# Optimization experiments

Measured on AMD Instinct MI355X. Metric: run time of the kernel, lower is better.

Reference implementation:

```python
import jax, jax.numpy as jnp
import numpy as np

ALPHA = 1.0
EPS = 1e-9
MASK_FILL = 100000.0  # large value pushes masked entries to the end of ascending sort


def setup_inputs() -> dict:
    key = jax.random.key(0)
    k1, k2, k3, k4 = jax.random.split(key, 4)
    bs, nh, n = 128, 32, 2048
    input1 = jax.random.normal(k1, (bs, 4, nh, n), dtype=jnp.float32)
    input2 = jax.random.normal(k2, (bs, 1, nh, n), dtype=jnp.float32)
    mask1 = jax.random.randint(k3, (bs, 4, nh, n), 0, 2).astype(jnp.int32)
    mask2 = jax.random.randint(k4, (bs, 1, nh, n), 0, 2).astype(jnp.int32)
    return {"input1": input1, "mask1": mask1, "input2": input2, "mask2": mask2}


def reference(input1, mask1, input2, mask2):
    # input1: (bs, 4, nh, n) scores; input2/mask2: (bs, 1, nh, n) targets/mask.
    # mask1 is unused by the original forward.
    i2 = jnp.where(mask2 > 0, input2, jnp.float32(MASK_FILL))
    idx = jnp.argsort(i2, axis=-1)                                  # (bs, 1, nh, n)
    mask_sorted = jnp.take_along_axis(mask2, idx, axis=-1).astype(jnp.float32)
    idx4 = jnp.broadcast_to(idx, input1.shape)                      # repeat over the 4 choices
    inputs_sorted = jnp.take_along_axis(input1, idx4, axis=-1)      # (bs, 4, nh, n)
    proj = jnp.exp(ALPHA * inputs_sorted) * mask_sorted             # mode='exp'
    proj_cum = jnp.cumsum(proj, axis=-1) * mask_sorted
    prob = jnp.prod((proj + EPS) / (proj_cum + EPS), axis=-1)       # (bs, 4, nh)
    return jnp.transpose(prob, (0, 2, 1))                           # (bs, nh, 4)
```

## Files before the change

kernel.cpp:

```cpp
#include <hip/hip_runtime.h>

#define N   2048
#define NT  128
#define EPK 16

typedef unsigned int u32;

__device__ __forceinline__ u32 fkey(float f) {
  u32 u = __float_as_uint(f);
  return (u & 0x80000000u) ? ~u : (u | 0x80000000u);
}

__device__ __forceinline__ u32 umin32(u32 a, u32 b) { return a < b ? a : b; }
__device__ __forceinline__ u32 umax32(u32 a, u32 b) { return a < b ? b : a; }

template <int D>
__device__ __forceinline__ u32 exch(u32 x, int lane) {
  if constexpr (D == 1) {
    return (u32)__builtin_amdgcn_update_dpp((int)x, (int)x, 0xB1, 0xF, 0xF, true);
  } else if constexpr (D == 2) {
    return (u32)__builtin_amdgcn_update_dpp((int)x, (int)x, 0x4E, 0xF, 0xF, true);
  } else if constexpr (D == 4) {
    return (u32)__builtin_amdgcn_ds_swizzle((int)x, 0x101F);
  } else if constexpr (D == 8) {
    return (u32)__builtin_amdgcn_update_dpp((int)x, (int)x, 0x128, 0xF, 0xF, true);
  } else if constexpr (D == 16) {
    return (u32)__builtin_amdgcn_ds_swizzle((int)x, 0x401F);
  } else {
    int a = (int)x, b = (int)x;
    asm("v_permlane32_swap_b32 %0, %1" : "+v"(a), "+v"(b));
    return (lane & 32) ? (u32)a : (u32)b;
  }
}

template <int D>
__device__ __forceinline__ void sh_pass(u32* kv, bool keep_min, int lane) {
#pragma unroll
  for (int m = 0; m < EPK; ++m) {
    u32 o = exch<D>(kv[m], lane);
    u32 mn = umin32(kv[m], o), mx = umax32(kv[m], o);
    kv[m] = keep_min ? mn : mx;
  }
}

#define INPASS(J, UPEXPR)                               \
  {                                                     \
    _Pragma("unroll")                                   \
    for (int m = 0; m < EPK; ++m)                       \
      if ((m & (J)) == 0) {                             \
        const bool up_ = (UPEXPR);                      \
        u32 x = kv[m], y = kv[m | (J)];                 \
        u32 mn = umin32(x, y), mx = umax32(x, y);       \
        kv[m] = up_ ? mn : mx;                          \
        kv[m | (J)] = up_ ? mx : mn;                    \
      }                                                 \
  }

__device__ __forceinline__ void stage_row(const float* __restrict__ r1,
                                          float* buf, int tid, int w) {
#pragma unroll
  for (int q = 0; q < 4; ++q) {
    const float4* src = (const float4*)r1 + (tid + 128 * q);
    char* dst = (char*)buf + q * 2048 + w * 1024;
    __builtin_amdgcn_global_load_lds(
        (const __attribute__((address_space(1))) unsigned int*)src,
        (__attribute__((address_space(3))) unsigned int*)dst, 16, 0, 0);
  }
}

__global__ __launch_bounds__(NT) void listmle_kernel(
    const float* __restrict__ input1,
    const float* __restrict__ input2,
    const int* __restrict__ mask2,
    float* __restrict__ out) {
  __shared__ __align__(16) float rowbuf[N];
  __shared__ __align__(16) u32 slab[N];
  __shared__ float hand[2];

  const int tid = threadIdx.x;
  const int lane = tid & 63;
  const int w = tid >> 6;
  const int p = blockIdx.x;
  const int b = p >> 5, h = p & 31;

  {
    const float4* i2v = (const float4*)(input2 + (size_t)p * N);
    const int4* m2v = (const int4*)(mask2 + (size_t)p * N);
#pragma unroll
    for (int q = 0; q < 4; ++q) {
      float4 vv = i2v[tid + 128 * q];
      int4 mm = m2v[tid + 128 * q];
      const u32 i0 = 4u * (u32)(tid + 128 * q);
      float vs[4] = {vv.x, vv.y, vv.z, vv.w};
      int ms[4] = {mm.x, mm.y, mm.z, mm.w};
#pragma unroll
      for (int r = 0; r < 4; ++r) {
        u32 idx = i0 + r;
        u32 key = (ms[r] > 0) ? ((fkey(vs[r]) & 0xFFFFF800u) | idx)
                              : (0xFFFFF800u | idx);
        slab[idx ^ ((idx >> 5) & 31u)] = key;
      }
    }
  }
  __syncthreads();
  u32 kv[EPK];
#pragma unroll
  for (int m = 0; m < EPK; ++m) {
    u32 idx = (u32)(w * 1024 + lane * EPK + m);
    kv[m] = slab[idx ^ ((idx >> 5) & 31u)];
  }

  stage_row(input1 + ((size_t)((b * 4 + 0) * 32 + h)) * N, rowbuf, tid, w);

  INPASS(1, (m & 2) == 0)
  INPASS(2, (m & 4) == 0) INPASS(1, (m & 4) == 0)
  INPASS(4, (m & 8) == 0) INPASS(2, (m & 8) == 0) INPASS(1, (m & 8) == 0)
  {
    const bool up = (lane & 1) == 0;
    INPASS(8, up) INPASS(4, up) INPASS(2, up) INPASS(1, up)
  }
  {
    const bool up = (lane & 2) == 0;
    sh_pass<1>(kv, ((lane & 1) == 0) == up, lane);
    INPASS(8, up) INPASS(4, up) INPASS(2, up) INPASS(1, up)
  }
  {
    const bool up = (lane & 4) == 0;
    sh_pass<2>(kv, ((lane & 2) == 0) == up, lane);
    sh_pass<1>(kv, ((lane & 1) == 0) == up, lane);
    INPASS(8, up) INPASS(4, up) INPASS(2, up) INPASS(1, up)
  }
  {
    const bool up = (lane & 8) == 0;
    sh_pass<4>(kv, ((lane & 4) == 0) == up, lane);
    sh_pass<2>(kv, ((lane & 2) == 0) == up, lane);
    sh_pass<1>(kv, ((lane & 1) == 0) == up, lane);
    INPASS(8, up) INPASS(4, up) INPASS(2, up) INPASS(1, up)
  }
  {
    const bool up = (lane & 16) == 0;
    sh_pass<8>(kv, ((lane & 8) == 0) == up, lane);
    sh_pass<4>(kv, ((lane & 4) == 0) == up, lane);
    sh_pass<2>(kv, ((lane & 2) == 0) == up, lane);
    sh_pass<1>(kv, ((lane & 1) == 0) == up, lane);
    INPASS(8, up) INPASS(4, up) INPASS(2, up) INPASS(1, up)
  }
  {
    const bool up = (lane & 32) == 0;
    sh_pass<16>(kv, ((lane & 16) == 0) == up, lane);
    sh_pass<8>(kv, ((lane & 8) == 0) == up, lane);
    sh_pass<4>(kv, ((lane & 4) == 0) == up, lane);
    sh_pass<2>(kv, ((lane & 2) == 0) == up, lane);
    sh_pass<1>(kv, ((lane & 1) == 0) == up, lane);
    INPASS(8, up) INPASS(4, up) INPASS(2, up) INPASS(1, up)
  }
  {
    const bool up = (w == 0);
    sh_pass<32>(kv, ((lane & 32) == 0) == up, lane);
    sh_pass<16>(kv, ((lane & 16) == 0) == up, lane);
    sh_pass<8>(kv, ((lane & 8) == 0) == up, lane);
    sh_pass<4>(kv, ((lane & 4) == 0) == up, lane);
    sh_pass<2>(kv, ((lane & 2) == 0) == up, lane);
    sh_pass<1>(kv, ((lane & 1) == 0) == up, lane);
    INPASS(8, up) INPASS(4, up) INPASS(2, up) INPASS(1, up)
  }
  {
    __syncthreads();
#pragma unroll
    for (int m = 0; m < EPK; ++m) slab[w * 1024 + m * 64 + lane] = kv[m];
    __syncthreads();
#pragma unroll
    for (int m = 0; m < EPK; ++m) {
      u32 o = slab[(w ^ 1) * 1024 + m * 64 + lane];
      kv[m] = (w == 0) ? umin32(kv[m], o) : umax32(kv[m], o);
    }
    __syncthreads();
    sh_pass<32>(kv, (lane & 32) == 0, lane);
    sh_pass<16>(kv, (lane & 16) == 0, lane);
    sh_pass<8>(kv, (lane & 8) == 0, lane);
    sh_pass<4>(kv, (lane & 4) == 0, lane);
    sh_pass<2>(kv, (lane & 2) == 0, lane);
    sh_pass<1>(kv, (lane & 1) == 0, lane);
    INPASS(8, true) INPASS(4, true) INPASS(2, true) INPASS(1, true)
  }

  u32 pk[EPK / 2];
#pragma unroll
  for (int t = 0; t < EPK / 2; ++t) {
    u32 a = kv[2 * t], b2 = kv[2 * t + 1];
    u32 ia = (a & 0x7FFu) | ((a < 0xFFFFF800u) ? 0x800u : 0u);
    u32 ib = (b2 & 0x7FFu) | ((b2 < 0xFFFFF800u) ? 0x800u : 0u);
    pk[t] = ia | (ib << 16);
  }

#pragma unroll
  for (int c = 0; c < 4; ++c) {
    float* buf = (c & 1) ? (float*)slab : rowbuf;
    __syncthreads();
    if (c < 3) {
      float* nbuf = (c & 1) ? rowbuf : (float*)slab;
      stage_row(input1 + ((size_t)((b * 4 + c + 1) * 32 + h)) * N, nbuf, tid, w);
    }

    float e[EPK];
    float lsum = 0.f;
#pragma unroll
    for (int m = 0; m < EPK; ++m) {
      u32 info = (pk[m >> 1] >> ((m & 1) * 16)) & 0xFFFFu;
      float v = buf[info & 0x7FFu];
      float pe = (info & 0x800u) ? __expf(v) : 0.f;
      e[m] = pe;
      lsum += pe;
    }

    float inc = lsum;
#pragma unroll
    for (int d = 1; d < 64; d <<= 1) {
      float o = __shfl_up(inc, d, 64);
      if (lane >= d) inc += o;
    }
    float excl = inc - lsum;

    if (w == 0) {
      float cum = excl;
      float prod = 1.f;
#pragma unroll
      for (int m = 0; m < EPK; ++m) {
        cum += e[m];
        u32 info = pk[m >> 1] >> ((m & 1) * 16);
        if (info & 0x800u) prod *= __fdividef(e[m] + 1e-9f, cum + 1e-9f);
      }
#pragma unroll
      for (int d = 1; d < 64; d <<= 1) prod *= __shfl_xor(prod, d, 64);
      if (lane == 63) hand[0] = inc;
      if (lane == 0) hand[1] = prod;
    }
    asm volatile("s_waitcnt lgkmcnt(0)" ::: "memory");
    __builtin_amdgcn_s_barrier();
    asm volatile("" ::: "memory");
    if (w == 1) {
      float cum = hand[0] + excl;
      float prod = 1.f;
#pragma unroll
      for (int m = 0; m < EPK; ++m) {
        cum += e[m];
        u32 info = pk[m >> 1] >> ((m & 1) * 16);
        if (info & 0x800u) prod *= __fdividef(e[m] + 1e-9f, cum + 1e-9f);
      }
#pragma unroll
      for (int d = 1; d < 64; d <<= 1) prod *= __shfl_xor(prod, d, 64);
      if (lane == 0) out[(size_t)p * 4 + c] = hand[1] * prod;
    }
  }
}

extern "C" void kernel_launch(void* const* d_in, const int* in_sizes, int n_in,
                              void* d_out, int out_size, void* d_ws, size_t ws_size,
                              hipStream_t stream) {
  const float* input1 = (const float*)d_in[0];
  const float* input2 = (const float*)d_in[2];
  const int* mask2 = (const int*)d_in[3];
  float* out = (float*)d_out;

  const int problems = 128 * 32;
  listmle_kernel<<<problems, NT, 0, stream>>>(input1, input2, mask2, out);
}
```

Baseline: 80.67 us.

## Split score rows across waves so each wave owns full sorted permutation

After the sort, the packed sorted-index pairs go through LDS so each wave holds the whole permutation, 32 entries per lane. Each wave then handles two of the four score rows independently, with its own LDS buffer and its own prefetch of the next row. This removes the per-row block barriers and the cross-wave handoff of prefix sums and partial products. In exchange each lane does twice as many exp/divide steps per row, uses more registers, and pays one extra LDS round trip for the permutation.

Result: faster. 76.38 us (-5.3%).

```diff
diff --git a/kernel.cpp b/kernel.cpp
--- a/kernel.cpp
+++ b/kernel.cpp
@@ -56,12 +56,12 @@
       }                                                 \
   }
 
-__device__ __forceinline__ void stage_row(const float* __restrict__ r1,
-                                          float* buf, int tid, int w) {
-#pragma unroll
-  for (int q = 0; q < 4; ++q) {
-    const float4* src = (const float4*)r1 + (tid + 128 * q);
-    char* dst = (char*)buf + q * 2048 + w * 1024;
+__device__ __forceinline__ void stage_row_full(const float* __restrict__ r1,
+                                               float* buf, int lane) {
+#pragma unroll
+  for (int q = 0; q < 8; ++q) {
+    const float4* src = (const float4*)r1 + (q * 64 + lane);
+    char* dst = (char*)buf + q * 1024;
     __builtin_amdgcn_global_load_lds(
         (const __attribute__((address_space(1))) unsigned int*)src,
         (__attribute__((address_space(3))) unsigned int*)dst, 16, 0, 0);
@@ -73,9 +73,8 @@
     const float* __restrict__ input2,
     const int* __restrict__ mask2,
     float* __restrict__ out) {
+  __shared__ __align__(16) u32 slab[N];
   __shared__ __align__(16) float rowbuf[N];
-  __shared__ __align__(16) u32 slab[N];
-  __shared__ float hand[2];
 
   const int tid = threadIdx.x;
   const int lane = tid & 63;
@@ -102,6 +101,10 @@
       }
     }
   }
+
+  if (w == 0)
+    stage_row_full(input1 + ((size_t)((b * 4 + 0) * 32 + h)) * N, rowbuf, lane);
+
   __syncthreads();
   u32 kv[EPK];
 #pragma unroll
@@ -109,8 +112,6 @@
     u32 idx = (u32)(w * 1024 + lane * EPK + m);
     kv[m] = slab[idx ^ ((idx >> 5) & 31u)];
   }
-
-  stage_row(input1 + ((size_t)((b * 4 + 0) * 32 + h)) * N, rowbuf, tid, w);
 
   INPASS(1, (m & 2) == 0)
   INPASS(2, (m & 4) == 0) INPASS(1, (m & 4) == 0)
@@ -184,73 +185,69 @@
     INPASS(8, true) INPASS(4, true) INPASS(2, true) INPASS(1, true)
   }
 
-  u32 pk[EPK / 2];
-#pragma unroll
-  for (int t = 0; t < EPK / 2; ++t) {
-    u32 a = kv[2 * t], b2 = kv[2 * t + 1];
-    u32 ia = (a & 0x7FFu) | ((a < 0xFFFFF800u) ? 0x800u : 0u);
-    u32 ib = (b2 & 0x7FFu) | ((b2 < 0xFFFFF800u) ? 0x800u : 0u);
-    pk[t] = ia | (ib << 16);
-  }
-
-#pragma unroll
-  for (int c = 0; c < 4; ++c) {
-    float* buf = (c & 1) ? (float*)slab : rowbuf;
-    __syncthreads();
-    if (c < 3) {
-      float* nbuf = (c & 1) ? rowbuf : (float*)slab;
-      stage_row(input1 + ((size_t)((b * 4 + c + 1) * 32 + h)) * N, nbuf, tid, w);
-    }
-
-    float e[EPK];
+  {
+    u32* pairs = slab;
+#pragma unroll
+    for (int t = 0; t < EPK / 2; ++t) {
+      u32 a = kv[2 * t], b2 = kv[2 * t + 1];
+      u32 ia = (a & 0x7FFu) | ((a < 0xFFFFF800u) ? 0x800u : 0u);
+      u32 ib = (b2 & 0x7FFu) | ((b2 < 0xFFFFF800u) ? 0x800u : 0u);
+      u32 slot = (u32)(w * 512 + lane * 8 + t);
+      pairs[slot ^ ((slot >> 5) & 31u)] = ia | (ib << 16);
+    }
+  }
+  __syncthreads();
+  u32 pk[EPK];
+#pragma unroll
+  for (int t = 0; t < EPK; ++t) {
+    u32 slot = (u32)(lane * 16 + t);
+    pk[t] = slab[slot ^ ((slot >> 5) & 31u)];
+  }
+  __syncthreads();
+
+  if (w == 1)
+    stage_row_full(input1 + ((size_t)((b * 4 + 2) * 32 + h)) * N, (float*)slab, lane);
+
+  float* mybuf = (w == 0) ? rowbuf : (float*)slab;
+#pragma unroll
+  for (int cc = 0; cc < 2; ++cc) {
+    const int c = 2 * w + cc;
+    asm volatile("s_waitcnt vmcnt(0)" ::: "memory");
+
+    float e[32];
     float lsum = 0.f;
 #pragma unroll
-    for (int m = 0; m < EPK; ++m) {
+    for (int m = 0; m < 32; ++m) {
       u32 info = (pk[m >> 1] >> ((m & 1) * 16)) & 0xFFFFu;
-      float v = buf[info & 0x7FFu];
+      float v = mybuf[info & 0x7FFu];
       float pe = (info & 0x800u) ? __expf(v) : 0.f;
       e[m] = pe;
       lsum += pe;
     }
 
+    if (cc == 0) {
+      asm volatile("s_waitcnt lgkmcnt(0)" ::: "memory");
+      stage_row_full(input1 + ((size_t)((b * 4 + c + 1) * 32 + h)) * N, mybuf, lane);
+    }
+
     float inc = lsum;
 #pragma unroll
     for (int d = 1; d < 64; d <<= 1) {
       float o = __shfl_up(inc, d, 64);
       if (lane >= d) inc += o;
     }
-    float excl = inc - lsum;
-
-    if (w == 0) {
-      float cum = excl;
-      float prod = 1.f;
-#pragma unroll
-      for (int m = 0; m < EPK; ++m) {
-        cum += e[m];
-        u32 info = pk[m >> 1] >> ((m & 1) * 16);
-        if (info & 0x800u) prod *= __fdividef(e[m] + 1e-9f, cum + 1e-9f);
-      }
-#pragma unroll
-      for (int d = 1; d < 64; d <<= 1) prod *= __shfl_xor(prod, d, 64);
-      if (lane == 63) hand[0] = inc;
-      if (lane == 0) hand[1] = prod;
-    }
-    asm volatile("s_waitcnt lgkmcnt(0)" ::: "memory");
-    __builtin_amdgcn_s_barrier();
-    asm volatile("" ::: "memory");
-    if (w == 1) {
-      float cum = hand[0] + excl;
-      float prod = 1.f;
-#pragma unroll
-      for (int m = 0; m < EPK; ++m) {
-        cum += e[m];
-        u32 info = pk[m >> 1] >> ((m & 1) * 16);
-        if (info & 0x800u) prod *= __fdividef(e[m] + 1e-9f, cum + 1e-9f);
-      }
-#pragma unroll
-      for (int d = 1; d < 64; d <<= 1) prod *= __shfl_xor(prod, d, 64);
-      if (lane == 0) out[(size_t)p * 4 + c] = hand[1] * prod;
-    }
+    float cum = inc - lsum;
+
+    float prod = 1.f;
+#pragma unroll
+    for (int m = 0; m < 32; ++m) {
+      cum += e[m];
+      u32 info = pk[m >> 1] >> ((m & 1) * 16);
+      if (info & 0x800u) prod *= __fdividef(e[m] + 1e-9f, cum + 1e-9f);
+    }
+#pragma unroll
+    for (int d = 1; d < 64; d <<= 1) prod *= __shfl_xor(prod, d, 64);
+    if (lane == 0) out[(size_t)p * 4 + c] = prod;
   }
 }
 
```
